# Performance work log

Hardware: AMD Instinct MI355X
Metric: run time of the kernel (lower is better)

The kernel has to match this reference:

```python
import jax, jax.numpy as jnp
import numpy as np
import math

KEY_SIZE = 64

def setup_inputs() -> dict:
    key = jax.random.key(0)
    kq, kk, kv, km = jax.random.split(key, 4)
    B, H, S, Dk, Dv = 4, 12, 2048, 64, 64
    Q = jax.random.normal(kq, (B, H, S, Dk), dtype=jnp.float32)
    K = jax.random.normal(kk, (B, H, S, Dk), dtype=jnp.float32)
    V = jax.random.normal(kv, (B, H, S, Dv), dtype=jnp.float32)
    mask_out = (jax.random.uniform(km, (B, H, 1, S)) < 0.9).astype(jnp.float32)
    return {"Q": Q, "K": K, "V": V, "mask_out": mask_out}

def reference(Q, K, V, mask_out):
    scale = math.sqrt(KEY_SIZE)
    # [B,H,Sq,Sk] scores
    scores = jnp.einsum('bhqd,bhkd->bhqk', Q, K) / scale
    attn = jax.nn.softmax(scores, axis=-1)
    attn = mask_out * attn  # post-softmax multiplicative mask (dropout=0)
    return jnp.einsum('bhqk,bhkv->bhqv', attn, V)
```

## Files before the change

### kernel.cpp

```cpp
#include <hip/hip_runtime.h>


typedef _Float16 f16x8 __attribute__((ext_vector_type(8)));
typedef _Float16 f16x4 __attribute__((ext_vector_type(4)));
typedef _Float16 f16x2 __attribute__((ext_vector_type(2)));
typedef float    f32x4 __attribute__((ext_vector_type(4)));

#define SEQ  2048
#define DIM  64
#define KT   64
#define LDSP 72
#define NIT  (SEQ / KT)

__device__ inline f16x8 cvt8(float4 a, float4 b) {
    return (f16x8){(_Float16)a.x,(_Float16)a.y,(_Float16)a.z,(_Float16)a.w,
                   (_Float16)b.x,(_Float16)b.y,(_Float16)b.z,(_Float16)b.w};
}
__device__ inline f16x8 cvt8s(float4 a, float4 b, float s) {
    return (f16x8){(_Float16)(a.x*s),(_Float16)(a.y*s),(_Float16)(a.z*s),(_Float16)(a.w*s),
                   (_Float16)(b.x*s),(_Float16)(b.y*s),(_Float16)(b.z*s),(_Float16)(b.w*s)};
}

__global__ __launch_bounds__(256, 3)
void fa_kernel(const float* __restrict__ Q, const float* __restrict__ K,
               const float* __restrict__ V, const float* __restrict__ Mask,
               float* __restrict__ Out)
{
    __shared__ _Float16 Kld[KT][LDSP];
    __shared__ _Float16 Vt[DIM][LDSP];

    const int bx    = blockIdx.x;
    const int head  = bx % 48;
    const int qtile = bx / 48;
    const int tid   = threadIdx.x;
    const int wave  = tid >> 6;
    const int lane  = tid & 63;
    const int quad  = lane >> 4;
    const int r     = lane & 15;

    const size_t hoff = (size_t)head * SEQ * DIM;
    const float* Qh = Q + hoff;
    const float* Kh = K + hoff;
    const float* Vh = V + hoff;
    const float* Mh = Mask + (size_t)head * SEQ;
    float* Oh = Out + hoff;

    const int qbase = qtile * 128 + wave * 32;
    const float c = 0.18033688011112042f;

    f16x8 qf[2][2];
    #pragma unroll
    for (int t = 0; t < 2; ++t) {
        const float* qrow = Qh + (size_t)(qbase + t * 16 + r) * DIM;
        #pragma unroll
        for (int kb = 0; kb < 2; ++kb) {
            const float4* p4 = (const float4*)(qrow + kb * 32 + quad * 8);
            qf[t][kb] = cvt8s(p4[0], p4[1], c);
        }
    }

    f32x4 o[4][2];
    float lsum[2] = {0.f, 0.f};
    #pragma unroll
    for (int d = 0; d < 4; ++d)
        #pragma unroll
        for (int t = 0; t < 2; ++t) o[d][t] = (f32x4){0.f, 0.f, 0.f, 0.f};

    const int skey = tid >> 2;
    const int sdb  = (tid & 3) * 16;
    const int vk0  = (tid & 31) * 2;
    const int vdb  = (tid >> 5) * 8;

    float4 kr0, kr1, kr2, kr3, va0, va1, vb0, vb1;
    float mk0, mk1;
    auto load_tile = [&](int kbase) {
        const float4* kg = (const float4*)(Kh + (size_t)(kbase + skey) * DIM + sdb);
        kr0 = kg[0]; kr1 = kg[1]; kr2 = kg[2]; kr3 = kg[3];
        const float4* vg0 = (const float4*)(Vh + (size_t)(kbase + vk0) * DIM + vdb);
        const float4* vg1 = (const float4*)(Vh + (size_t)(kbase + vk0 + 1) * DIM + vdb);
        va0 = vg0[0]; va1 = vg0[1];
        vb0 = vg1[0]; vb1 = vg1[1];
        mk0 = Mh[kbase + vk0]; mk1 = Mh[kbase + vk0 + 1];
    };
    load_tile(0);

    for (int kbi = 0; kbi < NIT; ++kbi) {
        __syncthreads();
        *(f16x8*)&Kld[skey][sdb]     = cvt8(kr0, kr1);
        *(f16x8*)&Kld[skey][sdb + 8] = cvt8(kr2, kr3);
        {
            float va[8] = {va0.x, va0.y, va0.z, va0.w, va1.x, va1.y, va1.z, va1.w};
            float vb[8] = {vb0.x, vb0.y, vb0.z, vb0.w, vb1.x, vb1.y, vb1.z, vb1.w};
            #pragma unroll
            for (int j = 0; j < 8; ++j) {
                f16x2 w = {(_Float16)(va[j] * mk0), (_Float16)(vb[j] * mk1)};
                *(f16x2*)&Vt[vdb + j][vk0] = w;
            }
        }
        __syncthreads();

        if (kbi + 1 < NIT) load_tile((kbi + 1) * KT);

        f16x4 pf[4][2];
        #pragma unroll
        for (int kt = 0; kt < 4; ++kt) {
            f16x8 kf0 = *(const f16x8*)&Kld[kt * 16 + r][0 * 32 + quad * 8];
            f16x8 kf1 = *(const f16x8*)&Kld[kt * 16 + r][1 * 32 + quad * 8];
            #pragma unroll
            for (int t = 0; t < 2; ++t) {
                f32x4 acc = (f32x4){-8.f, -8.f, -8.f, -8.f};
                acc = __builtin_amdgcn_mfma_f32_16x16x32_f16(kf0, qf[t][0], acc, 0, 0, 0);
                acc = __builtin_amdgcn_mfma_f32_16x16x32_f16(kf1, qf[t][1], acc, 0, 0, 0);
                float p0 = __builtin_amdgcn_exp2f(acc[0]);
                float p1 = __builtin_amdgcn_exp2f(acc[1]);
                float p2 = __builtin_amdgcn_exp2f(acc[2]);
                float p3 = __builtin_amdgcn_exp2f(acc[3]);
                lsum[t] += (p0 + p1) + (p2 + p3);
                pf[kt][t] = (f16x4){(_Float16)p0, (_Float16)p1,
                                    (_Float16)p2, (_Float16)p3};
            }
        }

        #pragma unroll
        for (int d = 0; d < 4; ++d) {
            #pragma unroll
            for (int kt = 0; kt < 4; ++kt) {
                f16x4 vfrag = *(const f16x4*)&Vt[d * 16 + r][kt * 16 + quad * 4];
                o[d][0] = __builtin_amdgcn_mfma_f32_16x16x16f16(vfrag, pf[kt][0], o[d][0], 0, 0, 0);
                o[d][1] = __builtin_amdgcn_mfma_f32_16x16x16f16(vfrag, pf[kt][1], o[d][1], 0, 0, 0);
            }
        }
    }

    #pragma unroll
    for (int t = 0; t < 2; ++t) {
        float l = lsum[t];
        l += __shfl_xor(l, 16);
        l += __shfl_xor(l, 32);
        float inv = 1.0f / l;
        const size_t rowoff = (size_t)(qbase + t * 16 + r) * DIM;
        #pragma unroll
        for (int d = 0; d < 4; ++d) {
            float4 v = {o[d][t][0] * inv, o[d][t][1] * inv,
                        o[d][t][2] * inv, o[d][t][3] * inv};
            *(float4*)&Oh[rowoff + d * 16 + quad * 4] = v;
        }
    }
}

extern "C" void kernel_launch(void* const* d_in, const int* in_sizes, int n_in,
                              void* d_out, int out_size, void* d_ws, size_t ws_size,
                              hipStream_t stream) {
    const float* Q = (const float*)d_in[0];
    const float* K = (const float*)d_in[1];
    const float* V = (const float*)d_in[2];
    const float* M = (const float*)d_in[3];
    float* O = (float*)d_out;
    dim3 grid(768), block(256);
    hipLaunchKernelGGL(fa_kernel, grid, block, 0, stream, Q, K, V, M, O);
}
```

Measured before the change: 176.3 us.

## Switch to 32x32x16 MFMA with double-buffered swizzled LDS and permlane P reshuffle

```diff
diff --git a/kernel.cpp b/kernel.cpp
--- a/kernel.cpp
+++ b/kernel.cpp
@@ -2,23 +2,42 @@
 
 
 typedef _Float16 f16x8 __attribute__((ext_vector_type(8)));
-typedef _Float16 f16x4 __attribute__((ext_vector_type(4)));
 typedef _Float16 f16x2 __attribute__((ext_vector_type(2)));
-typedef float    f32x4 __attribute__((ext_vector_type(4)));
+typedef float    f32x16 __attribute__((ext_vector_type(16)));
+typedef int      i32x2 __attribute__((ext_vector_type(2)));
+typedef int      i32x4 __attribute__((ext_vector_type(4)));
 
 #define SEQ  2048
 #define DIM  64
 #define KT   64
-#define LDSP 72
 #define NIT  (SEQ / KT)
 
-__device__ inline f16x8 cvt8(float4 a, float4 b) {
+__device__ __forceinline__ f16x8 cvt8(float4 a, float4 b) {
     return (f16x8){(_Float16)a.x,(_Float16)a.y,(_Float16)a.z,(_Float16)a.w,
                    (_Float16)b.x,(_Float16)b.y,(_Float16)b.z,(_Float16)b.w};
 }
-__device__ inline f16x8 cvt8s(float4 a, float4 b, float s) {
+__device__ __forceinline__ f16x8 cvt8s(float4 a, float4 b, float s) {
     return (f16x8){(_Float16)(a.x*s),(_Float16)(a.y*s),(_Float16)(a.z*s),(_Float16)(a.w*s),
                    (_Float16)(b.x*s),(_Float16)(b.y*s),(_Float16)(b.z*s),(_Float16)(b.w*s)};
+}
+__device__ __forceinline__ int pk2(float a, float b) {
+    f16x2 t = {(_Float16)a, (_Float16)b};
+    return __builtin_bit_cast(int, t);
+}
+__device__ __forceinline__ int swz(int row, int colh) {
+    return (row << 6) + (colh ^ ((row & 7) << 3));
+}
+__device__ __forceinline__ i32x2 plswap(int a, int b) {
+#if __has_builtin(__builtin_amdgcn_permlane32_swap)
+    return __builtin_amdgcn_permlane32_swap(a, b, false, false);
+#else
+    int ax = __shfl_xor(a, 32);
+    int bx = __shfl_xor(b, 32);
+    i32x2 r;
+    r[0] = (threadIdx.x & 32) ? bx : a;
+    r[1] = (threadIdx.x & 32) ? b  : ax;
+    return r;
+#endif
 }
 
 __global__ __launch_bounds__(256, 3)
@@ -26,8 +45,8 @@
                const float* __restrict__ V, const float* __restrict__ Mask,
                float* __restrict__ Out)
 {
-    __shared__ _Float16 Kld[KT][LDSP];
-    __shared__ _Float16 Vt[DIM][LDSP];
+    __shared__ __align__(16) _Float16 Kld[2][KT * DIM];
+    __shared__ __align__(16) _Float16 Vt [2][DIM * KT];
 
     const int bx    = blockIdx.x;
     const int head  = bx % 48;
@@ -35,8 +54,8 @@
     const int tid   = threadIdx.x;
     const int wave  = tid >> 6;
     const int lane  = tid & 63;
-    const int quad  = lane >> 4;
-    const int r     = lane & 15;
+    const int cl    = lane & 31;
+    const int hl    = lane >> 5;
 
     const size_t hoff = (size_t)head * SEQ * DIM;
     const float* Qh = Q + hoff;
@@ -48,23 +67,22 @@
     const int qbase = qtile * 128 + wave * 32;
     const float c = 0.18033688011112042f;
 
-    f16x8 qf[2][2];
+    f16x8 qf[4];
+    {
+        const float* qrow = Qh + (size_t)(qbase + cl) * DIM;
+        #pragma unroll
+        for (int kk = 0; kk < 4; ++kk) {
+            const float4* p4 = (const float4*)(qrow + kk * 16 + hl * 8);
+            qf[kk] = cvt8s(p4[0], p4[1], c);
+        }
+    }
+
+    f32x16 o[2];
     #pragma unroll
-    for (int t = 0; t < 2; ++t) {
-        const float* qrow = Qh + (size_t)(qbase + t * 16 + r) * DIM;
-        #pragma unroll
-        for (int kb = 0; kb < 2; ++kb) {
-            const float4* p4 = (const float4*)(qrow + kb * 32 + quad * 8);
-            qf[t][kb] = cvt8s(p4[0], p4[1], c);
-        }
-    }
-
-    f32x4 o[4][2];
-    float lsum[2] = {0.f, 0.f};
-    #pragma unroll
-    for (int d = 0; d < 4; ++d)
-        #pragma unroll
-        for (int t = 0; t < 2; ++t) o[d][t] = (f32x4){0.f, 0.f, 0.f, 0.f};
+    for (int dt = 0; dt < 2; ++dt)
+        #pragma unroll
+        for (int i = 0; i < 16; ++i) o[dt][i] = 0.f;
+    float lsum = 0.f;
 
     const int skey = tid >> 2;
     const int sdb  = (tid & 3) * 16;
@@ -82,68 +100,91 @@
         vb0 = vg1[0]; vb1 = vg1[1];
         mk0 = Mh[kbase + vk0]; mk1 = Mh[kbase + vk0 + 1];
     };
+    auto stage = [&](int b) {
+        *(f16x8*)&Kld[b][swz(skey, sdb)]     = cvt8(kr0, kr1);
+        *(f16x8*)&Kld[b][swz(skey, sdb + 8)] = cvt8(kr2, kr3);
+        float va[8] = {va0.x, va0.y, va0.z, va0.w, va1.x, va1.y, va1.z, va1.w};
+        float vb[8] = {vb0.x, vb0.y, vb0.z, vb0.w, vb1.x, vb1.y, vb1.z, vb1.w};
+        #pragma unroll
+        for (int j = 0; j < 8; ++j) {
+            f16x2 w = {(_Float16)(va[j] * mk0), (_Float16)(vb[j] * mk1)};
+            *(f16x2*)&Vt[b][swz(vdb + j, vk0)] = w;
+        }
+    };
+
     load_tile(0);
-
+    stage(0);
+    load_tile(KT);
+    __syncthreads();
+
+    int buf = 0;
     for (int kbi = 0; kbi < NIT; ++kbi) {
+        if (kbi + 1 < NIT) stage(buf ^ 1);
+        if (kbi + 2 < NIT) load_tile((kbi + 2) * KT);
+
+        #pragma unroll
+        for (int kt2 = 0; kt2 < 2; ++kt2) {
+            f16x8 kf[4];
+            #pragma unroll
+            for (int kk = 0; kk < 4; ++kk)
+                kf[kk] = *(const f16x8*)&Kld[buf][swz(kt2 * 32 + cl, kk * 16 + hl * 8)];
+
+            f32x16 acc;
+            #pragma unroll
+            for (int i = 0; i < 16; ++i) acc[i] = -8.f;
+            #pragma unroll
+            for (int kk = 0; kk < 4; ++kk)
+                acc = __builtin_amdgcn_mfma_f32_32x32x16_f16(kf[kk], qf[kk], acc, 0, 0, 0);
+
+            float p[16];
+            #pragma unroll
+            for (int i = 0; i < 16; ++i) p[i] = __builtin_amdgcn_exp2f(acc[i]);
+            {
+                float s0 = (p[0] + p[1])  + (p[2] + p[3]);
+                float s1 = (p[4] + p[5])  + (p[6] + p[7]);
+                float s2 = (p[8] + p[9])  + (p[10] + p[11]);
+                float s3 = (p[12] + p[13]) + (p[14] + p[15]);
+                lsum += (s0 + s1) + (s2 + s3);
+            }
+
+            f16x8 pf[2];
+            #pragma unroll
+            for (int ch = 0; ch < 2; ++ch) {
+                int x0 = pk2(p[8*ch + 0], p[8*ch + 1]);
+                int x1 = pk2(p[8*ch + 2], p[8*ch + 3]);
+                int y0 = pk2(p[8*ch + 4], p[8*ch + 5]);
+                int y1 = pk2(p[8*ch + 6], p[8*ch + 7]);
+                i32x2 s0 = plswap(x0, y0);
+                i32x2 s1 = plswap(x1, y1);
+                i32x4 w; w[0] = s0[0]; w[1] = s1[0]; w[2] = s0[1]; w[3] = s1[1];
+                pf[ch] = __builtin_bit_cast(f16x8, w);
+            }
+
+            #pragma unroll
+            for (int dt = 0; dt < 2; ++dt) {
+                #pragma unroll
+                for (int ch = 0; ch < 2; ++ch) {
+                    f16x8 vf = *(const f16x8*)&Vt[buf][swz(dt * 32 + cl,
+                                                           kt2 * 32 + ch * 16 + hl * 8)];
+                    o[dt] = __builtin_amdgcn_mfma_f32_32x32x16_f16(vf, pf[ch], o[dt], 0, 0, 0);
+                }
+            }
+        }
+
         __syncthreads();
-        *(f16x8*)&Kld[skey][sdb]     = cvt8(kr0, kr1);
-        *(f16x8*)&Kld[skey][sdb + 8] = cvt8(kr2, kr3);
-        {
-            float va[8] = {va0.x, va0.y, va0.z, va0.w, va1.x, va1.y, va1.z, va1.w};
-            float vb[8] = {vb0.x, vb0.y, vb0.z, vb0.w, vb1.x, vb1.y, vb1.z, vb1.w};
-            #pragma unroll
-            for (int j = 0; j < 8; ++j) {
-                f16x2 w = {(_Float16)(va[j] * mk0), (_Float16)(vb[j] * mk1)};
-                *(f16x2*)&Vt[vdb + j][vk0] = w;
-            }
-        }
-        __syncthreads();
-
-        if (kbi + 1 < NIT) load_tile((kbi + 1) * KT);
-
-        f16x4 pf[4][2];
-        #pragma unroll
-        for (int kt = 0; kt < 4; ++kt) {
-            f16x8 kf0 = *(const f16x8*)&Kld[kt * 16 + r][0 * 32 + quad * 8];
-            f16x8 kf1 = *(const f16x8*)&Kld[kt * 16 + r][1 * 32 + quad * 8];
-            #pragma unroll
-            for (int t = 0; t < 2; ++t) {
-                f32x4 acc = (f32x4){-8.f, -8.f, -8.f, -8.f};
-                acc = __builtin_amdgcn_mfma_f32_16x16x32_f16(kf0, qf[t][0], acc, 0, 0, 0);
-                acc = __builtin_amdgcn_mfma_f32_16x16x32_f16(kf1, qf[t][1], acc, 0, 0, 0);
-                float p0 = __builtin_amdgcn_exp2f(acc[0]);
-                float p1 = __builtin_amdgcn_exp2f(acc[1]);
-                float p2 = __builtin_amdgcn_exp2f(acc[2]);
-                float p3 = __builtin_amdgcn_exp2f(acc[3]);
-                lsum[t] += (p0 + p1) + (p2 + p3);
-                pf[kt][t] = (f16x4){(_Float16)p0, (_Float16)p1,
-                                    (_Float16)p2, (_Float16)p3};
-            }
-        }
-
-        #pragma unroll
-        for (int d = 0; d < 4; ++d) {
-            #pragma unroll
-            for (int kt = 0; kt < 4; ++kt) {
-                f16x4 vfrag = *(const f16x4*)&Vt[d * 16 + r][kt * 16 + quad * 4];
-                o[d][0] = __builtin_amdgcn_mfma_f32_16x16x16f16(vfrag, pf[kt][0], o[d][0], 0, 0, 0);
-                o[d][1] = __builtin_amdgcn_mfma_f32_16x16x16f16(vfrag, pf[kt][1], o[d][1], 0, 0, 0);
-            }
-        }
+        buf ^= 1;
     }
 
+    float l = lsum + __shfl_xor(lsum, 32);
+    float inv = 1.0f / l;
+    const size_t rowoff = (size_t)(qbase + cl) * DIM;
     #pragma unroll
-    for (int t = 0; t < 2; ++t) {
-        float l = lsum[t];
-        l += __shfl_xor(l, 16);
-        l += __shfl_xor(l, 32);
-        float inv = 1.0f / l;
-        const size_t rowoff = (size_t)(qbase + t * 16 + r) * DIM;
-        #pragma unroll
-        for (int d = 0; d < 4; ++d) {
-            float4 v = {o[d][t][0] * inv, o[d][t][1] * inv,
-                        o[d][t][2] * inv, o[d][t][3] * inv};
-            *(float4*)&Oh[rowoff + d * 16 + quad * 4] = v;
+    for (int dt = 0; dt < 2; ++dt) {
+        #pragma unroll
+        for (int g = 0; g < 4; ++g) {
+            float4 v = {o[dt][4*g + 0] * inv, o[dt][4*g + 1] * inv,
+                        o[dt][4*g + 2] * inv, o[dt][4*g + 3] * inv};
+            *(float4*)&Oh[rowoff + dt * 32 + g * 8 + hl * 4] = v;
         }
     }
 }
```

Result: slower. 193.5 us (+9.7%).

## Double-buffer K/V LDS tiles with XOR swizzle and one barrier per iteration

Applied to the files above, without the earlier changes.

```diff
diff --git a/kernel.cpp b/kernel.cpp
--- a/kernel.cpp
+++ b/kernel.cpp
@@ -9,25 +9,33 @@
 #define SEQ  2048
 #define DIM  64
 #define KT   64
-#define LDSP 72
 #define NIT  (SEQ / KT)
 
-__device__ inline f16x8 cvt8(float4 a, float4 b) {
+__device__ __forceinline__ f16x8 cvt8(float4 a, float4 b) {
     return (f16x8){(_Float16)a.x,(_Float16)a.y,(_Float16)a.z,(_Float16)a.w,
                    (_Float16)b.x,(_Float16)b.y,(_Float16)b.z,(_Float16)b.w};
 }
-__device__ inline f16x8 cvt8s(float4 a, float4 b, float s) {
+__device__ __forceinline__ f16x8 cvt8s(float4 a, float4 b, float s) {
     return (f16x8){(_Float16)(a.x*s),(_Float16)(a.y*s),(_Float16)(a.z*s),(_Float16)(a.w*s),
                    (_Float16)(b.x*s),(_Float16)(b.y*s),(_Float16)(b.z*s),(_Float16)(b.w*s)};
 }
+
+__device__ __forceinline__ int swz(int row, int colh) {
+    int super = row >> 1;
+    int blk   = ((row & 1) << 3) | (colh >> 3);
+    return (super << 7) + ((blk ^ (super & 15)) << 3) + (colh & 7);
+}
+
+#define BAR() do { asm volatile("s_waitcnt lgkmcnt(0)" ::: "memory"); \
+                   __builtin_amdgcn_s_barrier(); } while (0)
 
 __global__ __launch_bounds__(256, 3)
 void fa_kernel(const float* __restrict__ Q, const float* __restrict__ K,
                const float* __restrict__ V, const float* __restrict__ Mask,
                float* __restrict__ Out)
 {
-    __shared__ _Float16 Kld[KT][LDSP];
-    __shared__ _Float16 Vt[DIM][LDSP];
+    __shared__ __align__(16) _Float16 Kld[2][KT * DIM];
+    __shared__ __align__(16) _Float16 Vt [2][DIM * KT];
 
     const int bx    = blockIdx.x;
     const int head  = bx % 48;
@@ -82,35 +90,39 @@
         vb0 = vg1[0]; vb1 = vg1[1];
         mk0 = Mh[kbase + vk0]; mk1 = Mh[kbase + vk0 + 1];
     };
+    auto stage = [&](int b) {
+        *(f16x8*)&Kld[b][swz(skey, sdb)]     = cvt8(kr0, kr1);
+        *(f16x8*)&Kld[b][swz(skey, sdb + 8)] = cvt8(kr2, kr3);
+        _Float16* vt = &Vt[b][0];
+        #define VW(j, A, B) { f16x2 w = {(_Float16)((A) * mk0), (_Float16)((B) * mk1)}; \
+                              *(f16x2*)&vt[swz(vdb + (j), vk0)] = w; }
+        VW(0, va0.x, vb0.x) VW(1, va0.y, vb0.y) VW(2, va0.z, vb0.z) VW(3, va0.w, vb0.w)
+        VW(4, va1.x, vb1.x) VW(5, va1.y, vb1.y) VW(6, va1.z, vb1.z) VW(7, va1.w, vb1.w)
+        #undef VW
+    };
+
     load_tile(0);
+    stage(0);
+    load_tile(KT);
+    BAR();
 
+    int buf = 0;
     for (int kbi = 0; kbi < NIT; ++kbi) {
-        __syncthreads();
-        *(f16x8*)&Kld[skey][sdb]     = cvt8(kr0, kr1);
-        *(f16x8*)&Kld[skey][sdb + 8] = cvt8(kr2, kr3);
-        {
-            float va[8] = {va0.x, va0.y, va0.z, va0.w, va1.x, va1.y, va1.z, va1.w};
-            float vb[8] = {vb0.x, vb0.y, vb0.z, vb0.w, vb1.x, vb1.y, vb1.z, vb1.w};
-            #pragma unroll
-            for (int j = 0; j < 8; ++j) {
-                f16x2 w = {(_Float16)(va[j] * mk0), (_Float16)(vb[j] * mk1)};
-                *(f16x2*)&Vt[vdb + j][vk0] = w;
-            }
-        }
-        __syncthreads();
-
-        if (kbi + 1 < NIT) load_tile((kbi + 1) * KT);
+        if (kbi + 1 < NIT) stage(buf ^ 1);
+        if (kbi + 2 < NIT) load_tile((kbi + 2) * KT);
 
         f16x4 pf[4][2];
         #pragma unroll
         for (int kt = 0; kt < 4; ++kt) {
-            f16x8 kf0 = *(const f16x8*)&Kld[kt * 16 + r][0 * 32 + quad * 8];
-            f16x8 kf1 = *(const f16x8*)&Kld[kt * 16 + r][1 * 32 + quad * 8];
+            f16x8 kf0 = *(const f16x8*)&Kld[buf][swz(kt * 16 + r, quad * 8)];
+            f16x8 kf1 = *(const f16x8*)&Kld[buf][swz(kt * 16 + r, 32 + quad * 8)];
             #pragma unroll
             for (int t = 0; t < 2; ++t) {
                 f32x4 acc = (f32x4){-8.f, -8.f, -8.f, -8.f};
+                __builtin_amdgcn_s_setprio(1);
                 acc = __builtin_amdgcn_mfma_f32_16x16x32_f16(kf0, qf[t][0], acc, 0, 0, 0);
                 acc = __builtin_amdgcn_mfma_f32_16x16x32_f16(kf1, qf[t][1], acc, 0, 0, 0);
+                __builtin_amdgcn_s_setprio(0);
                 float p0 = __builtin_amdgcn_exp2f(acc[0]);
                 float p1 = __builtin_amdgcn_exp2f(acc[1]);
                 float p2 = __builtin_amdgcn_exp2f(acc[2]);
@@ -121,15 +133,20 @@
             }
         }
 
+        __builtin_amdgcn_s_setprio(1);
         #pragma unroll
         for (int d = 0; d < 4; ++d) {
             #pragma unroll
             for (int kt = 0; kt < 4; ++kt) {
-                f16x4 vfrag = *(const f16x4*)&Vt[d * 16 + r][kt * 16 + quad * 4];
+                f16x4 vfrag = *(const f16x4*)&Vt[buf][swz(d * 16 + r, kt * 16 + quad * 4)];
                 o[d][0] = __builtin_amdgcn_mfma_f32_16x16x16f16(vfrag, pf[kt][0], o[d][0], 0, 0, 0);
                 o[d][1] = __builtin_amdgcn_mfma_f32_16x16x16f16(vfrag, pf[kt][1], o[d][1], 0, 0, 0);
             }
         }
+        __builtin_amdgcn_s_setprio(0);
+
+        BAR();
+        buf ^= 1;
     }
 
     #pragma unroll
```

Measured after the change: 338.6 us. +92.1%, slower.
